# Kernel optimization log

Measured on AMD Instinct MI355X. Metric: run time of the kernel, lower is better.

The kernel has to match this reference:

```python
import jax, jax.numpy as jnp
import numpy as np


def setup_inputs() -> dict:
    key = jax.random.key(0)
    ks = jax.random.split(key, 10)
    N, CZ, CH = 512, 128, 128
    s = 1.0 / np.sqrt(CZ)  # keep pre-sigmoid activations in a sane range
    return {
        "z": jax.random.normal(ks[0], (N, N, CZ), dtype=jnp.float32),
        "mask": jnp.ones((N, N, 1), dtype=jnp.float32),
        "weight_ag": jax.random.normal(ks[1], (CH, CZ), dtype=jnp.float32) * s,
        "bias_ag": jax.random.normal(ks[2], (CH,), dtype=jnp.float32) * 0.02,
        "weight_ap": jax.random.normal(ks[3], (CH, CZ), dtype=jnp.float32) * s,
        "bias_ap": jax.random.normal(ks[4], (CH,), dtype=jnp.float32) * 0.02,
        "weight_bg": jax.random.normal(ks[5], (CH, CZ), dtype=jnp.float32) * s,
        "bias_bg": jax.random.normal(ks[6], (CH,), dtype=jnp.float32) * 0.02,
        "weight_bp": jax.random.normal(ks[7], (CH, CZ), dtype=jnp.float32) * s,
        "bias_bp": jax.random.normal(ks[8], (CH,), dtype=jnp.float32) * 0.02,
        "chunk_size": 32,
    }


def _triangle_mul(z, mask, w_ag, b_ag, w_ap, b_ap, w_bg, b_bg, w_bp, b_bp):
    # z: [N, N, c_z]; mask: [N, N, 1]; weights: [c, c_z]
    # a = mask * sigmoid(Linear_ag(z)) * Linear_ap(z)   -> [N, N, c]
    a = mask * jax.nn.sigmoid(jnp.einsum("ijz,cz->ijc", z, w_ag) + b_ag) * (
        jnp.einsum("ijz,cz->ijc", z, w_ap) + b_ap
    )
    b = mask * jax.nn.sigmoid(jnp.einsum("ijz,cz->ijc", z, w_bg) + b_bg) * (
        jnp.einsum("ijz,cz->ijc", z, w_bp) + b_bp
    )
    # outgoing triangle multiplicative combination, channel-first output [c, N, N]
    return jnp.einsum("ikc,jkc->cij", a, b)


def reference(z, mask, weight_ag, bias_ag, weight_ap, bias_ap,
              weight_bg, bias_bg, weight_bp, bias_bp, chunk_size):
    # The torch wrapper chunks the hidden-channel dim of the weights and
    # concatenates the per-chunk [c, N, N] outputs along dim 0. Since every
    # channel is independent, this is mathematically identical to running the
    # full computation at once; we do that (clean, fused form).
    return _triangle_mul(z, mask, weight_ag, bias_ag, weight_ap, bias_ap,
                         weight_bg, bias_bg, weight_bp, bias_bp)
```

## Files before the change

kernel.cpp:

```cpp
#include <hip/hip_runtime.h>
#include <stdint.h>


#define NDIM 512
#define CZ   128
#define CH   128
#define NPOS (NDIM * NDIM)

typedef __attribute__((ext_vector_type(8))) __bf16 bf16x8;
typedef __attribute__((ext_vector_type(4))) float  f32x4;

__device__ __forceinline__ unsigned short f2bf(float f) {
  unsigned int u = __builtin_bit_cast(unsigned int, f);
  unsigned int r = (u + 0x7fffu + ((u >> 16) & 1u)) >> 16;
  return (unsigned short)r;
}

__global__ __launch_bounds__(256) void conv_weights(
    const float* __restrict__ wag, const float* __restrict__ wap,
    const float* __restrict__ wbg, const float* __restrict__ wbp,
    unsigned short* __restrict__ wbf) {
  int idx = blockIdx.x * 256 + threadIdx.x;
  int proj = idx >> 14;
  int rem  = idx & 16383;
  const float* src = (proj == 0) ? wag : (proj == 1) ? wap : (proj == 2) ? wbg : wbp;
  wbf[idx] = f2bf(src[rem]);
}

__global__ __launch_bounds__(256) void proj_fuse(
    const float* __restrict__ z,
    const float* __restrict__ mask,
    const unsigned short* __restrict__ wbf,
    const float* __restrict__ bias_ag, const float* __restrict__ bias_ap,
    const float* __restrict__ bias_bg, const float* __restrict__ bias_bp,
    unsigned short* __restrict__ a_ws,
    unsigned short* __restrict__ b_ws) {
  __shared__ unsigned short sbuf[128 * 72];

  const int t    = threadIdx.x;
  const int lane = t & 63;
  const int wave = t >> 6;
  const int wm   = wave >> 1;
  const int wn   = wave & 1;
  const int m0   = blockIdx.x * 64;
  const int pair = blockIdx.y;

  {
    const int col4  = t & 31;
    const int rbase = t >> 5;
    for (int it = 0; it < 8; ++it) {
      const int row = it * 8 + rbase;
      const float4 v = *(const float4*)(z + (size_t)(m0 + row) * CZ + col4 * 4);
      unsigned int lo = (unsigned int)f2bf(v.x) | ((unsigned int)f2bf(v.y) << 16);
      unsigned int hi = (unsigned int)f2bf(v.z) | ((unsigned int)f2bf(v.w) << 16);
      *(uint2*)&sbuf[row * 136 + col4 * 4] = make_uint2(lo, hi);
    }
  }
  __syncthreads();

  const int pg = pair * 2;
  const int pp = pg + 1;

  f32x4 accg[2][4], accp[2][4];
  for (int mi = 0; mi < 2; ++mi)
    for (int ni = 0; ni < 4; ++ni) {
      accg[mi][ni] = (f32x4){0.f, 0.f, 0.f, 0.f};
      accp[mi][ni] = (f32x4){0.f, 0.f, 0.f, 0.f};
    }

  const int mrow  = wm * 32 + (lane & 15);
  const int nrow  = wn * 64 + (lane & 15);
  const int koffl = (lane >> 4) * 8;

  for (int ks = 0; ks < 4; ++ks) {
    bf16x8 af[2];
    af[0] = *(const bf16x8*)&sbuf[(mrow)      * 136 + ks * 32 + koffl];
    af[1] = *(const bf16x8*)&sbuf[(mrow + 16) * 136 + ks * 32 + koffl];
#pragma unroll
    for (int ni = 0; ni < 4; ++ni) {
      const int c = nrow + ni * 16;
      bf16x8 bg = *(const bf16x8*)&wbf[(pg * CH + c) * CZ + ks * 32 + koffl];
      bf16x8 bp = *(const bf16x8*)&wbf[(pp * CH + c) * CZ + ks * 32 + koffl];
      accg[0][ni] = __builtin_amdgcn_mfma_f32_16x16x32_bf16(af[0], bg, accg[0][ni], 0, 0, 0);
      accg[1][ni] = __builtin_amdgcn_mfma_f32_16x16x32_bf16(af[1], bg, accg[1][ni], 0, 0, 0);
      accp[0][ni] = __builtin_amdgcn_mfma_f32_16x16x32_bf16(af[0], bp, accp[0][ni], 0, 0, 0);
      accp[1][ni] = __builtin_amdgcn_mfma_f32_16x16x32_bf16(af[1], bp, accp[1][ni], 0, 0, 0);
    }
  }
  __syncthreads();

  const float* bgp = pair ? bias_bg : bias_ag;
  const float* bpp = pair ? bias_bp : bias_ap;

  float mk[2][4];
  for (int mi = 0; mi < 2; ++mi)
    for (int r = 0; r < 4; ++r)
      mk[mi][r] = mask[m0 + wm * 32 + mi * 16 + (lane >> 4) * 4 + r];

#pragma unroll
  for (int ni = 0; ni < 4; ++ni) {
    const int c = nrow + ni * 16;
    const float bgv = bgp[c];
    const float bpv = bpp[c];
#pragma unroll
    for (int mi = 0; mi < 2; ++mi) {
      unsigned short h[4];
#pragma unroll
      for (int r = 0; r < 4; ++r) {
        float g = accg[mi][ni][r] + bgv;
        float p = accp[mi][ni][r] + bpv;
        float s = 1.0f / (1.0f + __expf(-g));
        h[r] = f2bf(mk[mi][r] * s * p);
      }
      const int mloc = wm * 32 + mi * 16 + (lane >> 4) * 4;
      *(uint2*)&sbuf[c * 72 + mloc] =
          make_uint2((unsigned int)h[0] | ((unsigned int)h[1] << 16),
                     (unsigned int)h[2] | ((unsigned int)h[3] << 16));
    }
  }
  __syncthreads();

  unsigned short* plane = pair ? b_ws : a_ws;
  {
    const int p4 = t & 15;
    const int cb = t >> 4;
    for (int it = 0; it < 8; ++it) {
      const int c = it * 16 + cb;
      uint2 v = *(const uint2*)&sbuf[c * 72 + p4 * 4];
      *(uint2*)(plane + (size_t)c * NPOS + m0 + p4 * 4) = v;
    }
  }
}

__global__ __launch_bounds__(256) void tri_gemm(
    const unsigned short* __restrict__ a_ws,
    const unsigned short* __restrict__ b_ws,
    float* __restrict__ out) {
  __shared__ unsigned short sA[128 * 32];
  __shared__ unsigned short sB[128 * 32];

  const int t = threadIdx.x, lane = t & 63, wave = t >> 6;
  const int wm = wave >> 1, wn = wave & 1;
  const int tj = blockIdx.x, ti = blockIdx.y, c = blockIdx.z;
  const int i0 = ti * 128, j0 = tj * 128;

  const unsigned short* Ap = a_ws + (size_t)c * NPOS + (size_t)i0 * NDIM;
  const unsigned short* Bp = b_ws + (size_t)c * NPOS + (size_t)j0 * NDIM;

  f32x4 acc[4][4];
  for (int mi = 0; mi < 4; ++mi)
    for (int ni = 0; ni < 4; ++ni) acc[mi][ni] = (f32x4){0.f, 0.f, 0.f, 0.f};

  const int srow  = t >> 2;
  const int scol  = t & 3;
  const int mrow  = wm * 64 + (lane & 15);
  const int nrow  = wn * 64 + (lane & 15);
  const int koffl = (lane >> 4) * 8;

  for (int kk = 0; kk < 16; ++kk) {
    const int k0 = kk * 32;
    __builtin_amdgcn_global_load_lds(
        (const __attribute__((address_space(1))) unsigned int*)(Ap + (size_t)srow * NDIM + k0 + scol * 8),
        (__attribute__((address_space(3))) unsigned int*)&sA[t * 8], 16, 0, 0);
    __builtin_amdgcn_global_load_lds(
        (const __attribute__((address_space(1))) unsigned int*)(Ap + (size_t)(srow + 64) * NDIM + k0 + scol * 8),
        (__attribute__((address_space(3))) unsigned int*)&sA[2048 + t * 8], 16, 0, 0);
    __builtin_amdgcn_global_load_lds(
        (const __attribute__((address_space(1))) unsigned int*)(Bp + (size_t)srow * NDIM + k0 + scol * 8),
        (__attribute__((address_space(3))) unsigned int*)&sB[t * 8], 16, 0, 0);
    __builtin_amdgcn_global_load_lds(
        (const __attribute__((address_space(1))) unsigned int*)(Bp + (size_t)(srow + 64) * NDIM + k0 + scol * 8),
        (__attribute__((address_space(3))) unsigned int*)&sB[2048 + t * 8], 16, 0, 0);
    __syncthreads();

    bf16x8 af[4], bfr[4];
#pragma unroll
    for (int mi = 0; mi < 4; ++mi)
      af[mi] = *(const bf16x8*)&sA[(mrow + mi * 16) * 32 + koffl];
#pragma unroll
    for (int ni = 0; ni < 4; ++ni)
      bfr[ni] = *(const bf16x8*)&sB[(nrow + ni * 16) * 32 + koffl];
#pragma unroll
    for (int mi = 0; mi < 4; ++mi)
#pragma unroll
      for (int ni = 0; ni < 4; ++ni)
        acc[mi][ni] = __builtin_amdgcn_mfma_f32_16x16x32_bf16(af[mi], bfr[ni], acc[mi][ni], 0, 0, 0);
    __syncthreads();
  }

  float* O = out + (size_t)c * NPOS + (size_t)i0 * NDIM + j0;
#pragma unroll
  for (int mi = 0; mi < 4; ++mi)
#pragma unroll
    for (int r = 0; r < 4; ++r) {
      const int m = wm * 64 + mi * 16 + (lane >> 4) * 4 + r;
#pragma unroll
      for (int ni = 0; ni < 4; ++ni) {
        const int n = wn * 64 + ni * 16 + (lane & 15);
        O[(size_t)m * NDIM + n] = acc[mi][ni][r];
      }
    }
}

extern "C" void kernel_launch(void* const* d_in, const int* in_sizes, int n_in,
                              void* d_out, int out_size, void* d_ws, size_t ws_size,
                              hipStream_t stream) {
  const float* z    = (const float*)d_in[0];
  const float* mask = (const float*)d_in[1];
  const float* wag  = (const float*)d_in[2];
  const float* bag  = (const float*)d_in[3];
  const float* wap  = (const float*)d_in[4];
  const float* bap  = (const float*)d_in[5];
  const float* wbg  = (const float*)d_in[6];
  const float* bbg  = (const float*)d_in[7];
  const float* wbp  = (const float*)d_in[8];
  const float* bbp  = (const float*)d_in[9];
  float* out = (float*)d_out;

  unsigned short* wbf  = (unsigned short*)d_ws;
  unsigned short* a_ws = (unsigned short*)((char*)d_ws + 131072);
  unsigned short* b_ws = (unsigned short*)((char*)d_ws + 131072 + (size_t)CH * NPOS * 2);

  conv_weights<<<dim3(256), dim3(256), 0, stream>>>(wag, wap, wbg, wbp, wbf);
  proj_fuse<<<dim3(NPOS / 64, 2), dim3(256), 0, stream>>>(
      z, mask, wbf, bag, bap, bbg, bbp, a_ws, b_ws);
  tri_gemm<<<dim3(4, 4, CH), dim3(256), 0, stream>>>(a_ws, b_ws, out);
}
```

Before: 449.9 us.

## Persist projection weights in registers, prefetch z tiles, widen GEMM K-tile with swizzle

proj_fuse now has each block process four 64-position tiles. It keeps the bf16 weight fragments in registers across those tiles and prefetches the next z tile into registers while the current tile computes. This is meant to cut repeated weight loads and hide global load latency, at the cost of much higher register use. tri_gemm doubles the K tile to 64 and uses an XOR-swizzled LDS layout, which halves the barrier count and reduces LDS bank conflicts. Launch-bound occupancy hints are added to both kernels.

Result: faster. 435.0 us (-3.3%).

```diff
diff --git a/kernel.cpp b/kernel.cpp
--- a/kernel.cpp
+++ b/kernel.cpp
@@ -6,6 +6,7 @@
 #define CZ   128
 #define CH   128
 #define NPOS (NDIM * NDIM)
+#define TILES 4
 
 typedef __attribute__((ext_vector_type(8))) __bf16 bf16x8;
 typedef __attribute__((ext_vector_type(4))) float  f32x4;
@@ -27,7 +28,7 @@
   wbf[idx] = f2bf(src[rem]);
 }
 
-__global__ __launch_bounds__(256) void proj_fuse(
+__global__ __launch_bounds__(256, 2) void proj_fuse(
     const float* __restrict__ z,
     const float* __restrict__ mask,
     const unsigned short* __restrict__ wbf,
@@ -35,109 +36,132 @@
     const float* __restrict__ bias_bg, const float* __restrict__ bias_bp,
     unsigned short* __restrict__ a_ws,
     unsigned short* __restrict__ b_ws) {
-  __shared__ unsigned short sbuf[128 * 72];
+  __shared__ unsigned short zbuf[64 * 136];
+  __shared__ unsigned short tbuf[128 * 72];
 
   const int t    = threadIdx.x;
   const int lane = t & 63;
   const int wave = t >> 6;
   const int wm   = wave >> 1;
   const int wn   = wave & 1;
-  const int m0   = blockIdx.x * 64;
   const int pair = blockIdx.y;
-
-  {
-    const int col4  = t & 31;
-    const int rbase = t >> 5;
-    for (int it = 0; it < 8; ++it) {
-      const int row = it * 8 + rbase;
-      const float4 v = *(const float4*)(z + (size_t)(m0 + row) * CZ + col4 * 4);
-      unsigned int lo = (unsigned int)f2bf(v.x) | ((unsigned int)f2bf(v.y) << 16);
-      unsigned int hi = (unsigned int)f2bf(v.z) | ((unsigned int)f2bf(v.w) << 16);
-      *(uint2*)&sbuf[row * 136 + col4 * 4] = make_uint2(lo, hi);
-    }
-  }
-  __syncthreads();
-
-  const int pg = pair * 2;
-  const int pp = pg + 1;
-
-  f32x4 accg[2][4], accp[2][4];
-  for (int mi = 0; mi < 2; ++mi)
-    for (int ni = 0; ni < 4; ++ni) {
-      accg[mi][ni] = (f32x4){0.f, 0.f, 0.f, 0.f};
-      accp[mi][ni] = (f32x4){0.f, 0.f, 0.f, 0.f};
-    }
+  const int pg   = pair * 2, pp = pg + 1;
 
   const int mrow  = wm * 32 + (lane & 15);
   const int nrow  = wn * 64 + (lane & 15);
   const int koffl = (lane >> 4) * 8;
 
-  for (int ks = 0; ks < 4; ++ks) {
-    bf16x8 af[2];
-    af[0] = *(const bf16x8*)&sbuf[(mrow)      * 136 + ks * 32 + koffl];
-    af[1] = *(const bf16x8*)&sbuf[(mrow + 16) * 136 + ks * 32 + koffl];
+  bf16x8 wg[4][4], wp[4][4];
+#pragma unroll
+  for (int ks = 0; ks < 4; ++ks)
 #pragma unroll
     for (int ni = 0; ni < 4; ++ni) {
       const int c = nrow + ni * 16;
-      bf16x8 bg = *(const bf16x8*)&wbf[(pg * CH + c) * CZ + ks * 32 + koffl];
-      bf16x8 bp = *(const bf16x8*)&wbf[(pp * CH + c) * CZ + ks * 32 + koffl];
-      accg[0][ni] = __builtin_amdgcn_mfma_f32_16x16x32_bf16(af[0], bg, accg[0][ni], 0, 0, 0);
-      accg[1][ni] = __builtin_amdgcn_mfma_f32_16x16x32_bf16(af[1], bg, accg[1][ni], 0, 0, 0);
-      accp[0][ni] = __builtin_amdgcn_mfma_f32_16x16x32_bf16(af[0], bp, accp[0][ni], 0, 0, 0);
-      accp[1][ni] = __builtin_amdgcn_mfma_f32_16x16x32_bf16(af[1], bp, accp[1][ni], 0, 0, 0);
-    }
-  }
-  __syncthreads();
+      wg[ks][ni] = *(const bf16x8*)&wbf[(pg * CH + c) * CZ + ks * 32 + koffl];
+      wp[ks][ni] = *(const bf16x8*)&wbf[(pp * CH + c) * CZ + ks * 32 + koffl];
+    }
 
   const float* bgp = pair ? bias_bg : bias_ag;
   const float* bpp = pair ? bias_bp : bias_ap;
-
-  float mk[2][4];
-  for (int mi = 0; mi < 2; ++mi)
-    for (int r = 0; r < 4; ++r)
-      mk[mi][r] = mask[m0 + wm * 32 + mi * 16 + (lane >> 4) * 4 + r];
-
-#pragma unroll
-  for (int ni = 0; ni < 4; ++ni) {
-    const int c = nrow + ni * 16;
-    const float bgv = bgp[c];
-    const float bpv = bpp[c];
-#pragma unroll
-    for (int mi = 0; mi < 2; ++mi) {
-      unsigned short h[4];
-#pragma unroll
-      for (int r = 0; r < 4; ++r) {
-        float g = accg[mi][ni][r] + bgv;
-        float p = accp[mi][ni][r] + bpv;
-        float s = 1.0f / (1.0f + __expf(-g));
-        h[r] = f2bf(mk[mi][r] * s * p);
-      }
-      const int mloc = wm * 32 + mi * 16 + (lane >> 4) * 4;
-      *(uint2*)&sbuf[c * 72 + mloc] =
-          make_uint2((unsigned int)h[0] | ((unsigned int)h[1] << 16),
-                     (unsigned int)h[2] | ((unsigned int)h[3] << 16));
+  unsigned short* plane = pair ? b_ws : a_ws;
+
+  const int col4  = t & 31;
+  const int rbase = t >> 5;
+
+  const int m0 = blockIdx.x * (TILES * 64);
+
+  float4 zf[8];
+#pragma unroll
+  for (int it = 0; it < 8; ++it)
+    zf[it] = *(const float4*)(z + (size_t)(m0 + it * 8 + rbase) * CZ + col4 * 4);
+
+  for (int tt = 0; tt < TILES; ++tt) {
+    const int mt = m0 + tt * 64;
+
+#pragma unroll
+    for (int it = 0; it < 8; ++it) {
+      const int row = it * 8 + rbase;
+      unsigned int lo = (unsigned int)f2bf(zf[it].x) | ((unsigned int)f2bf(zf[it].y) << 16);
+      unsigned int hi = (unsigned int)f2bf(zf[it].z) | ((unsigned int)f2bf(zf[it].w) << 16);
+      *(uint2*)&zbuf[row * 136 + col4 * 4] = make_uint2(lo, hi);
+    }
+    __syncthreads();
+
+    if (tt + 1 < TILES) {
+#pragma unroll
+      for (int it = 0; it < 8; ++it)
+        zf[it] = *(const float4*)(z + (size_t)(mt + 64 + it * 8 + rbase) * CZ + col4 * 4);
+    }
+    float mk[2][4];
+#pragma unroll
+    for (int mi = 0; mi < 2; ++mi)
+#pragma unroll
+      for (int r = 0; r < 4; ++r)
+        mk[mi][r] = mask[mt + wm * 32 + mi * 16 + (lane >> 4) * 4 + r];
+
+    f32x4 accg[2][4], accp[2][4];
+#pragma unroll
+    for (int mi = 0; mi < 2; ++mi)
+#pragma unroll
+      for (int ni = 0; ni < 4; ++ni) {
+        accg[mi][ni] = (f32x4){0.f, 0.f, 0.f, 0.f};
+        accp[mi][ni] = (f32x4){0.f, 0.f, 0.f, 0.f};
+      }
+#pragma unroll
+    for (int ks = 0; ks < 4; ++ks) {
+      bf16x8 af0 = *(const bf16x8*)&zbuf[(mrow)      * 136 + ks * 32 + koffl];
+      bf16x8 af1 = *(const bf16x8*)&zbuf[(mrow + 16) * 136 + ks * 32 + koffl];
+#pragma unroll
+      for (int ni = 0; ni < 4; ++ni) {
+        accg[0][ni] = __builtin_amdgcn_mfma_f32_16x16x32_bf16(af0, wg[ks][ni], accg[0][ni], 0, 0, 0);
+        accg[1][ni] = __builtin_amdgcn_mfma_f32_16x16x32_bf16(af1, wg[ks][ni], accg[1][ni], 0, 0, 0);
+        accp[0][ni] = __builtin_amdgcn_mfma_f32_16x16x32_bf16(af0, wp[ks][ni], accp[0][ni], 0, 0, 0);
+        accp[1][ni] = __builtin_amdgcn_mfma_f32_16x16x32_bf16(af1, wp[ks][ni], accp[1][ni], 0, 0, 0);
+      }
+    }
+
+#pragma unroll
+    for (int ni = 0; ni < 4; ++ni) {
+      const int c = nrow + ni * 16;
+      const float bgv = bgp[c];
+      const float bpv = bpp[c];
+#pragma unroll
+      for (int mi = 0; mi < 2; ++mi) {
+        unsigned short h[4];
+#pragma unroll
+        for (int r = 0; r < 4; ++r) {
+          float g = accg[mi][ni][r] + bgv;
+          float p = accp[mi][ni][r] + bpv;
+          float s = 1.0f / (1.0f + __expf(-g));
+          h[r] = f2bf(mk[mi][r] * s * p);
+        }
+        const int mloc = wm * 32 + mi * 16 + (lane >> 4) * 4;
+        *(uint2*)&tbuf[c * 72 + mloc] =
+            make_uint2((unsigned int)h[0] | ((unsigned int)h[1] << 16),
+                       (unsigned int)h[2] | ((unsigned int)h[3] << 16));
+      }
+    }
+    __syncthreads();
+
+    {
+      const int p4 = t & 15;
+      const int cb = t >> 4;
+#pragma unroll
+      for (int it = 0; it < 8; ++it) {
+        const int c = it * 16 + cb;
+        uint2 v = *(const uint2*)&tbuf[c * 72 + p4 * 4];
+        *(uint2*)(plane + (size_t)c * NPOS + mt + p4 * 4) = v;
+      }
     }
   }
-  __syncthreads();
-
-  unsigned short* plane = pair ? b_ws : a_ws;
-  {
-    const int p4 = t & 15;
-    const int cb = t >> 4;
-    for (int it = 0; it < 8; ++it) {
-      const int c = it * 16 + cb;
-      uint2 v = *(const uint2*)&sbuf[c * 72 + p4 * 4];
-      *(uint2*)(plane + (size_t)c * NPOS + m0 + p4 * 4) = v;
-    }
-  }
-}
-
-__global__ __launch_bounds__(256) void tri_gemm(
+}
+
+__global__ __launch_bounds__(256, 3) void tri_gemm(
     const unsigned short* __restrict__ a_ws,
     const unsigned short* __restrict__ b_ws,
     float* __restrict__ out) {
-  __shared__ unsigned short sA[128 * 32];
-  __shared__ unsigned short sB[128 * 32];
+  __shared__ unsigned short sA[128 * 64];
+  __shared__ unsigned short sB[128 * 64];
 
   const int t = threadIdx.x, lane = t & 63, wave = t >> 6;
   const int wm = wave >> 1, wn = wave & 1;
@@ -148,43 +172,51 @@
   const unsigned short* Bp = b_ws + (size_t)c * NPOS + (size_t)j0 * NDIM;
 
   f32x4 acc[4][4];
+#pragma unroll
   for (int mi = 0; mi < 4; ++mi)
+#pragma unroll
     for (int ni = 0; ni < 4; ++ni) acc[mi][ni] = (f32x4){0.f, 0.f, 0.f, 0.f};
 
-  const int srow  = t >> 2;
-  const int scol  = t & 3;
-  const int mrow  = wm * 64 + (lane & 15);
-  const int nrow  = wn * 64 + (lane & 15);
-  const int koffl = (lane >> 4) * 8;
-
-  for (int kk = 0; kk < 16; ++kk) {
-    const int k0 = kk * 32;
-    __builtin_amdgcn_global_load_lds(
-        (const __attribute__((address_space(1))) unsigned int*)(Ap + (size_t)srow * NDIM + k0 + scol * 8),
-        (__attribute__((address_space(3))) unsigned int*)&sA[t * 8], 16, 0, 0);
-    __builtin_amdgcn_global_load_lds(
-        (const __attribute__((address_space(1))) unsigned int*)(Ap + (size_t)(srow + 64) * NDIM + k0 + scol * 8),
-        (__attribute__((address_space(3))) unsigned int*)&sA[2048 + t * 8], 16, 0, 0);
-    __builtin_amdgcn_global_load_lds(
-        (const __attribute__((address_space(1))) unsigned int*)(Bp + (size_t)srow * NDIM + k0 + scol * 8),
-        (__attribute__((address_space(3))) unsigned int*)&sB[t * 8], 16, 0, 0);
-    __builtin_amdgcn_global_load_lds(
-        (const __attribute__((address_space(1))) unsigned int*)(Bp + (size_t)(srow + 64) * NDIM + k0 + scol * 8),
-        (__attribute__((address_space(3))) unsigned int*)&sB[2048 + t * 8], 16, 0, 0);
-    __syncthreads();
-
-    bf16x8 af[4], bfr[4];
-#pragma unroll
-    for (int mi = 0; mi < 4; ++mi)
-      af[mi] = *(const bf16x8*)&sA[(mrow + mi * 16) * 32 + koffl];
-#pragma unroll
-    for (int ni = 0; ni < 4; ++ni)
-      bfr[ni] = *(const bf16x8*)&sB[(nrow + ni * 16) * 32 + koffl];
-#pragma unroll
-    for (int mi = 0; mi < 4; ++mi)
-#pragma unroll
-      for (int ni = 0; ni < 4; ++ni)
-        acc[mi][ni] = __builtin_amdgcn_mfma_f32_16x16x32_bf16(af[mi], bfr[ni], acc[mi][ni], 0, 0, 0);
+  const int srow8  = t >> 3;
+  const int schunk = t & 7;
+  const int mrow = wm * 64 + (lane & 15);
+  const int nrow = wn * 64 + (lane & 15);
+
+  for (int kk = 0; kk < 8; ++kk) {
+    const int k0 = kk * 64;
+#pragma unroll
+    for (int i = 0; i < 4; ++i) {
+      const int row = i * 32 + srow8;
+      const int kcs = schunk ^ (row & 7);
+      __builtin_amdgcn_global_load_lds(
+          (const __attribute__((address_space(1))) unsigned int*)(Ap + (size_t)row * NDIM + k0 + kcs * 8),
+          (__attribute__((address_space(3))) unsigned int*)&sA[(i * 256 + t) * 8], 16, 0, 0);
+      __builtin_amdgcn_global_load_lds(
+          (const __attribute__((address_space(1))) unsigned int*)(Bp + (size_t)row * NDIM + k0 + kcs * 8),
+          (__attribute__((address_space(3))) unsigned int*)&sB[(i * 256 + t) * 8], 16, 0, 0);
+    }
+    __syncthreads();
+
+#pragma unroll
+    for (int ksub = 0; ksub < 2; ++ksub) {
+      const int kc = ksub * 4 + (lane >> 4);
+      bf16x8 af[4], bfr[4];
+#pragma unroll
+      for (int mi = 0; mi < 4; ++mi) {
+        const int r = mrow + mi * 16;
+        af[mi] = *(const bf16x8*)&sA[r * 64 + ((kc ^ (r & 7)) << 3)];
+      }
+#pragma unroll
+      for (int ni = 0; ni < 4; ++ni) {
+        const int r = nrow + ni * 16;
+        bfr[ni] = *(const bf16x8*)&sB[r * 64 + ((kc ^ (r & 7)) << 3)];
+      }
+#pragma unroll
+      for (int mi = 0; mi < 4; ++mi)
+#pragma unroll
+        for (int ni = 0; ni < 4; ++ni)
+          acc[mi][ni] = __builtin_amdgcn_mfma_f32_16x16x32_bf16(af[mi], bfr[ni], acc[mi][ni], 0, 0, 0);
+    }
     __syncthreads();
   }
 
@@ -222,7 +254,7 @@
   unsigned short* b_ws = (unsigned short*)((char*)d_ws + 131072 + (size_t)CH * NPOS * 2);
 
   conv_weights<<<dim3(256), dim3(256), 0, stream>>>(wag, wap, wbg, wbp, wbf);
-  proj_fuse<<<dim3(NPOS / 64, 2), dim3(256), 0, stream>>>(
+  proj_fuse<<<dim3(NPOS / (64 * TILES), 2), dim3(256), 0, stream>>>(
       z, mask, wbf, bag, bap, bbg, bbp, a_ws, b_ws);
   tri_gemm<<<dim3(4, 4, CH), dim3(256), 0, stream>>>(a_ws, b_ws, out);
 }
```
